# Kernel optimization log

Measured on AMD Instinct MI355X. Metric: run time of the kernel, lower is better.

## Reference

```python
import jax, jax.numpy as jnp
import numpy as np

B, N, H, E, D = 8, 2048, 1024, 8, 2048


def setup_inputs() -> dict:
    key = jax.random.key(0)
    k = jax.random.split(key, 5)
    x = jax.random.normal(k[0], (B, N, H), dtype=jnp.float32)
    Wr = jax.random.normal(k[1], (H, E), dtype=jnp.float32) * 0.02
    br = jnp.zeros((E,), dtype=jnp.float32)
    W1 = jax.random.normal(k[2], (E, H, D), dtype=jnp.float32) * 0.02
    b1 = jnp.zeros((E, D), dtype=jnp.float32)
    W2 = jax.random.normal(k[3], (E, D, H), dtype=jnp.float32) * 0.02
    b2 = jnp.zeros((E, H), dtype=jnp.float32)
    return {"x": x, "Wr": Wr, "br": br, "W1": W1, "b1": b1, "W2": W2, "b2": b2}


def reference(x, Wr, br, W1, b1, W2, b2):
    # x: [B,N,H]; router v1, top-1, eval mode (no expert dropout)
    Bx, Nx, Hx = x.shape
    Ex = Wr.shape[1]
    x_flat = x.reshape(Bx * Nx, Hx)                      # [T,H]
    logits = x_flat @ Wr + br                            # [T,E]
    probs = jax.nn.softmax(logits, axis=-1)              # [T,E]
    expert_idx = jnp.argmax(probs, axis=-1)              # [T]

    out_flat = jnp.zeros_like(x_flat)
    for e in range(Ex):  # small fixed loop over experts
        h = jax.nn.gelu(x_flat @ W1[e] + b1[e], approximate=False)  # exact erf GELU (torch default)
        eout = h @ W2[e] + b2[e]                         # [T,H]
        out_flat = jnp.where((expert_idx == e)[:, None], eout, out_flat)

    out = x + out_flat.reshape(Bx, Nx, Hx)               # residual

    p_i = probs.mean(axis=0)                             # [E]
    balance_loss = Ex * jnp.sum(p_i ** 2)
    EPS = 1e-8
    entropy = -jnp.sum(probs * jnp.log(probs + EPS), axis=-1)
    entropy_loss = entropy.mean()
    tokens_per_expert = jnp.bincount(expert_idx, length=Ex)
    return out, balance_loss, entropy_loss, tokens_per_expert
```

## Files before the change

kernel.cpp:

```cpp
#include <hip/hip_runtime.h>
#include <math.h>

#define TT 16384
#define HH 1024
#define DD 2048
#define EE 8
#define MAXTILES 160

typedef float f32x4 __attribute__((ext_vector_type(4)));
typedef __bf16 bf16x8 __attribute__((ext_vector_type(8)));

__device__ __forceinline__ unsigned short f2bf(float f) {
  union { float f; unsigned u; } v; v.f = f;
  unsigned r = v.u + 0x7FFFu + ((v.u >> 16) & 1u);
  return (unsigned short)(r >> 16);
}

__device__ __forceinline__ void gl2lds16(const unsigned short* g, unsigned short* l) {
  __builtin_amdgcn_global_load_lds(
      (const __attribute__((address_space(1))) void*)g,
      (__attribute__((address_space(3))) void*)l, 16, 0, 0);
}

__global__ void k_init(int* counts, float* probs_sum, float* ent_sum) {
  int t = threadIdx.x;
  if (t < EE) { counts[t] = 0; probs_sum[t] = 0.f; }
  if (t == 0) *ent_sum = 0.f;
}

__global__ __launch_bounds__(256) void k_transpose(const float* __restrict__ src,
                                                   unsigned short* __restrict__ dst,
                                                   int R, int C) {
  __shared__ float tile[32][33];
  int tilesC = C / 32, tilesR = R / 32;
  int bid = blockIdx.x;
  int e = bid / (tilesR * tilesC);
  int rem = bid % (tilesR * tilesC);
  int tr = rem / tilesC, tc = rem % tilesC;
  const float* s = src + (size_t)e * R * C;
  unsigned short* d = dst + (size_t)e * R * C;
  int tx = threadIdx.x & 31, ty = threadIdx.x >> 5;
#pragma unroll
  for (int i = 0; i < 4; ++i)
    tile[ty + i * 8][tx] = s[(size_t)(tr * 32 + ty + i * 8) * C + tc * 32 + tx];
  __syncthreads();
#pragma unroll
  for (int i = 0; i < 4; ++i) {
    int rr = ty + i * 8;
    d[(size_t)(tc * 32 + rr) * R + tr * 32 + tx] = f2bf(tile[tx][rr]);
  }
}

__global__ __launch_bounds__(256) void k_router(const float* __restrict__ x,
                                                const float* __restrict__ Wr,
                                                const float* __restrict__ br,
                                                int* __restrict__ eidx,
                                                float* __restrict__ probs_sum,
                                                float* __restrict__ ent_sum,
                                                int* __restrict__ counts,
                                                unsigned short* __restrict__ xb) {
  __shared__ float s_p[EE];
  __shared__ int   s_c[EE];
  __shared__ float s_e;
  int tid = threadIdx.x;
  if (tid < EE) { s_p[tid] = 0.f; s_c[tid] = 0; }
  if (tid == 0) s_e = 0.f;
  __syncthreads();
  int lane = tid & 63, w = tid >> 6;
  for (int tt = 0; tt < 4; ++tt) {
    int token = blockIdx.x * 16 + w * 4 + tt;
    double acc[EE];
#pragma unroll
    for (int e = 0; e < EE; ++e) acc[e] = 0.0;
    const float* xr = x + (size_t)token * HH;
    unsigned short* xo = xb + (size_t)token * HH;
    for (int i = 0; i < 16; ++i) {
      int hh = i * 64 + lane;
      float xf = xr[hh];
      xo[hh] = f2bf(xf);
      double xv = (double)xf;
      const float* wr = Wr + (size_t)hh * EE;
#pragma unroll
      for (int e = 0; e < EE; ++e) acc[e] += xv * (double)wr[e];
    }
#pragma unroll
    for (int off = 32; off > 0; off >>= 1) {
#pragma unroll
      for (int e = 0; e < EE; ++e) acc[e] += __shfl_down(acc[e], off);
    }
    if (lane == 0) {
      double l[EE];
#pragma unroll
      for (int e = 0; e < EE; ++e) l[e] = acc[e] + (double)br[e];
      double m = l[0]; int am = 0;
#pragma unroll
      for (int e = 1; e < EE; ++e) { if (l[e] > m) { m = l[e]; am = e; } }
      double p[EE]; double s = 0.0;
#pragma unroll
      for (int e = 0; e < EE; ++e) { p[e] = exp(l[e] - m); s += p[e]; }
      double inv = 1.0 / s; double ent = 0.0;
#pragma unroll
      for (int e = 0; e < EE; ++e) { p[e] *= inv; ent -= p[e] * log(p[e] + 1e-8); }
      eidx[token] = am;
#pragma unroll
      for (int e = 0; e < EE; ++e) atomicAdd(&s_p[e], (float)p[e]);
      atomicAdd(&s_e, (float)ent);
      atomicAdd(&s_c[am], 1);
    }
  }
  __syncthreads();
  if (tid < EE) { atomicAdd(&probs_sum[tid], s_p[tid]); atomicAdd(&counts[tid], s_c[tid]); }
  if (tid == 0) atomicAdd(ent_sum, s_e);
}

__global__ void k_scan(const int* counts, const float* probs_sum, const float* ent_sum,
                       int* offsets, int* cursor,
                       int* tileE, int* tileR0, int* tileEnd, int* nTiles,
                       float* out_scalars) {
  if (threadIdx.x != 0) return;
  int off = 0, nt = 0;
  for (int e = 0; e < EE; ++e) {
    offsets[e] = off; cursor[e] = off;
    int c = counts[e];
    for (int r = 0; r < c; r += 128) {
      tileE[nt] = e; tileR0[nt] = off + r; tileEnd[nt] = off + c; ++nt;
    }
    off += c;
  }
  offsets[EE] = off;
  *nTiles = nt;
  float bal = 0.f;
  for (int e = 0; e < EE; ++e) { float pi = probs_sum[e] / (float)TT; bal += pi * pi; }
  out_scalars[0] = (float)EE * bal;
  out_scalars[1] = *ent_sum / (float)TT;
  for (int e = 0; e < EE; ++e) out_scalars[2 + e] = (float)counts[e];
}

__global__ __launch_bounds__(256) void k_perm(const int* __restrict__ eidx,
                                              int* cursor, int* __restrict__ perm) {
  int t = blockIdx.x * 256 + threadIdx.x;
  int lane = threadIdx.x & 63;
  int mye = eidx[t];
  int pos = 0;
#pragma unroll
  for (int e = 0; e < EE; ++e) {
    unsigned long long mask = __ballot(mye == e);
    if (mask == 0ull) continue;
    int leader = __ffsll(mask) - 1;
    int base = 0;
    if (lane == leader) base = atomicAdd(&cursor[e], __popcll(mask));
    base = __shfl(base, leader);
    if (mye == e) pos = base + (int)__popcll(mask & ((1ull << lane) - 1ull));
  }
  perm[pos] = t;
}


__global__ __launch_bounds__(256) void k_gemm1(const unsigned short* __restrict__ xb,
                                               const unsigned short* __restrict__ Wt1,
                                               const float* __restrict__ b1,
                                               const int* __restrict__ perm,
                                               const int* __restrict__ tileE,
                                               const int* __restrict__ tileR0,
                                               const int* __restrict__ tileEnd,
                                               const int* __restrict__ nTiles,
                                               unsigned short* __restrict__ hbuf) {
  int tile = blockIdx.y;
  if (tile >= *nTiles) return;
  int e = tileE[tile], r0 = tileR0[tile], rend = tileEnd[tile];
  int c0 = blockIdx.x * 128;
  __shared__ __align__(16) unsigned short As[128 * 32];
  __shared__ __align__(16) unsigned short Bs[128 * 32];
  int tid = threadIdx.x, lane = tid & 63, w = tid >> 6;
  int wr = w >> 1, wc = w & 1;
  int quad = lane >> 4, l16 = lane & 15;
  int srow = lane >> 2, seg = lane & 3;
  int ar0 = w * 32 + srow, ar1 = ar0 + 16;
  int g0 = r0 + ar0; if (g0 >= rend) g0 = rend - 1;
  int g1 = r0 + ar1; if (g1 >= rend) g1 = rend - 1;
  const unsigned short* aG0 = xb + (size_t)perm[g0] * HH + seg * 8;
  const unsigned short* aG1 = xb + (size_t)perm[g1] * HH + seg * 8;
  const unsigned short* bBase = Wt1 + (size_t)e * ((size_t)DD * HH);
  const unsigned short* bG0 = bBase + (size_t)(c0 + ar0) * HH + seg * 8;
  const unsigned short* bG1 = bBase + (size_t)(c0 + ar1) * HH + seg * 8;
  unsigned short* aL0 = &As[(w * 32 + 0) * 32];
  unsigned short* aL1 = &As[(w * 32 + 16) * 32];
  unsigned short* bL0 = &Bs[(w * 32 + 0) * 32];
  unsigned short* bL1 = &Bs[(w * 32 + 16) * 32];
  f32x4 acc[4][4] = {};
  for (int k0 = 0; k0 < HH; k0 += 32) {
    gl2lds16(aG0 + k0, aL0);
    gl2lds16(aG1 + k0, aL1);
    gl2lds16(bG0 + k0, bL0);
    gl2lds16(bG1 + k0, bL1);
    __syncthreads();
    bf16x8 a[4], b[4];
#pragma unroll
    for (int i = 0; i < 4; ++i)
      a[i] = *(const bf16x8*)&As[(wr * 64 + i * 16 + l16) * 32 + quad * 8];
#pragma unroll
    for (int j = 0; j < 4; ++j)
      b[j] = *(const bf16x8*)&Bs[(wc * 64 + j * 16 + l16) * 32 + quad * 8];
#pragma unroll
    for (int i = 0; i < 4; ++i)
#pragma unroll
      for (int j = 0; j < 4; ++j)
        acc[i][j] = __builtin_amdgcn_mfma_f32_16x16x32_bf16(a[i], b[j], acc[i][j], 0, 0, 0);
    __syncthreads();
  }
  float bias[4];
#pragma unroll
  for (int j = 0; j < 4; ++j) bias[j] = b1[e * DD + c0 + wc * 64 + j * 16 + l16];
#pragma unroll
  for (int i = 0; i < 4; ++i) {
#pragma unroll
    for (int r = 0; r < 4; ++r) {
      int gr = r0 + wr * 64 + i * 16 + quad * 4 + r;
      if (gr < rend) {
#pragma unroll
        for (int j = 0; j < 4; ++j) {
          int col = c0 + wc * 64 + j * 16 + l16;
          float v = acc[i][j][r] + bias[j];
          v = 0.5f * v * (1.0f + erff(v * 0.70710678118654752f));
          hbuf[(size_t)gr * DD + col] = f2bf(v);
        }
      }
    }
  }
}

__global__ __launch_bounds__(256) void k_gemm2(const unsigned short* __restrict__ hbuf,
                                               const unsigned short* __restrict__ Wt2,
                                               const float* __restrict__ b2,
                                               const float* __restrict__ x,
                                               const int* __restrict__ perm,
                                               const int* __restrict__ tileE,
                                               const int* __restrict__ tileR0,
                                               const int* __restrict__ tileEnd,
                                               const int* __restrict__ nTiles,
                                               float* __restrict__ outp) {
  int tile = blockIdx.y;
  if (tile >= *nTiles) return;
  int e = tileE[tile], r0 = tileR0[tile], rend = tileEnd[tile];
  int c0 = blockIdx.x * 128;
  __shared__ __align__(16) unsigned short As[128 * 32];
  __shared__ __align__(16) unsigned short Bs[128 * 32];
  int tid = threadIdx.x, lane = tid & 63, w = tid >> 6;
  int wr = w >> 1, wc = w & 1;
  int quad = lane >> 4, l16 = lane & 15;
  int srow = lane >> 2, seg = lane & 3;
  int ar0 = w * 32 + srow, ar1 = ar0 + 16;
  int g0 = r0 + ar0; if (g0 >= rend) g0 = rend - 1;
  int g1 = r0 + ar1; if (g1 >= rend) g1 = rend - 1;
  const unsigned short* aG0 = hbuf + (size_t)g0 * DD + seg * 8;
  const unsigned short* aG1 = hbuf + (size_t)g1 * DD + seg * 8;
  const unsigned short* bBase = Wt2 + (size_t)e * ((size_t)HH * DD);
  const unsigned short* bG0 = bBase + (size_t)(c0 + ar0) * DD + seg * 8;
  const unsigned short* bG1 = bBase + (size_t)(c0 + ar1) * DD + seg * 8;
  unsigned short* aL0 = &As[(w * 32 + 0) * 32];
  unsigned short* aL1 = &As[(w * 32 + 16) * 32];
  unsigned short* bL0 = &Bs[(w * 32 + 0) * 32];
  unsigned short* bL1 = &Bs[(w * 32 + 16) * 32];
  f32x4 acc[4][4] = {};
  for (int k0 = 0; k0 < DD; k0 += 32) {
    gl2lds16(aG0 + k0, aL0);
    gl2lds16(aG1 + k0, aL1);
    gl2lds16(bG0 + k0, bL0);
    gl2lds16(bG1 + k0, bL1);
    __syncthreads();
    bf16x8 a[4], b[4];
#pragma unroll
    for (int i = 0; i < 4; ++i)
      a[i] = *(const bf16x8*)&As[(wr * 64 + i * 16 + l16) * 32 + quad * 8];
#pragma unroll
    for (int j = 0; j < 4; ++j)
      b[j] = *(const bf16x8*)&Bs[(wc * 64 + j * 16 + l16) * 32 + quad * 8];
#pragma unroll
    for (int i = 0; i < 4; ++i)
#pragma unroll
      for (int j = 0; j < 4; ++j)
        acc[i][j] = __builtin_amdgcn_mfma_f32_16x16x32_bf16(a[i], b[j], acc[i][j], 0, 0, 0);
    __syncthreads();
  }
  float bias[4];
#pragma unroll
  for (int j = 0; j < 4; ++j) bias[j] = b2[e * HH + c0 + wc * 64 + j * 16 + l16];
#pragma unroll
  for (int i = 0; i < 4; ++i) {
#pragma unroll
    for (int r = 0; r < 4; ++r) {
      int gr = r0 + wr * 64 + i * 16 + quad * 4 + r;
      if (gr < rend) {
        int tok = perm[gr];
#pragma unroll
        for (int j = 0; j < 4; ++j) {
          int col = c0 + wc * 64 + j * 16 + l16;
          size_t oi = (size_t)tok * HH + col;
          outp[oi] = x[oi] + bias[j] + acc[i][j][r];
        }
      }
    }
  }
}

extern "C" void kernel_launch(void* const* d_in, const int* in_sizes, int n_in,
                              void* d_out, int out_size, void* d_ws, size_t ws_size,
                              hipStream_t stream) {
  const float* x  = (const float*)d_in[0];
  const float* Wr = (const float*)d_in[1];
  const float* br = (const float*)d_in[2];
  const float* W1 = (const float*)d_in[3];
  const float* b1 = (const float*)d_in[4];
  const float* W2 = (const float*)d_in[5];
  const float* b2 = (const float*)d_in[6];
  float* outp = (float*)d_out;

  char* ws = (char*)d_ws;
  int*   counts    = (int*)(ws + 0);
  int*   cursor    = (int*)(ws + 64);
  int*   nTiles    = (int*)(ws + 128);
  float* probs_sum = (float*)(ws + 192);
  float* ent_sum   = (float*)(ws + 256);
  int*   offsets   = (int*)(ws + 320);
  int*   tileE     = (int*)(ws + 512);
  int*   tileR0    = (int*)(ws + 2048);
  int*   tileEnd   = (int*)(ws + 3584);
  int*   eidx      = (int*)(ws + 8192);
  int*   perm      = (int*)(ws + 8192 + 4 * (size_t)TT);
  size_t off = 8192 + 8 * (size_t)TT;
  unsigned short* xb   = (unsigned short*)(ws + off); off += (size_t)TT * HH * 2;
  unsigned short* Wt1  = (unsigned short*)(ws + off); off += (size_t)EE * DD * HH * 2;
  unsigned short* Wt2  = (unsigned short*)(ws + off); off += (size_t)EE * HH * DD * 2;
  unsigned short* hbuf = (unsigned short*)(ws + off); off += (size_t)TT * DD * 2;

  k_init<<<1, 64, 0, stream>>>(counts, probs_sum, ent_sum);
  k_transpose<<<EE * (HH / 32) * (DD / 32), 256, 0, stream>>>(W1, Wt1, HH, DD);
  k_transpose<<<EE * (DD / 32) * (HH / 32), 256, 0, stream>>>(W2, Wt2, DD, HH);
  k_router<<<TT / 16, 256, 0, stream>>>(x, Wr, br, eidx, probs_sum, ent_sum, counts, xb);
  k_scan<<<1, 64, 0, stream>>>(counts, probs_sum, ent_sum, offsets, cursor,
                               tileE, tileR0, tileEnd, nTiles, outp + (size_t)TT * HH);
  k_perm<<<TT / 256, 256, 0, stream>>>(eidx, cursor, perm);
  dim3 g1(DD / 128, MAXTILES);
  k_gemm1<<<g1, 256, 0, stream>>>(xb, Wt1, b1, perm, tileE, tileR0, tileEnd, nTiles, hbuf);
  dim3 g2(HH / 128, MAXTILES);
  k_gemm2<<<g2, 256, 0, stream>>>(hbuf, Wt2, b2, x, perm, tileE, tileR0, tileEnd, nTiles, outp);
}
```

Measured before the change: 598.3 us.

## Widen GEMM tiles to 128x256 with 512 threads, vectorize transpose and router

Both expert GEMMs now use 128x256 output tiles computed by 8 waves, so each A tile staged in LDS is reused across twice as many columns. The aim is to cut redundant global and L2 traffic on the activation rows. The weight transpose kernel now uses 64x64 tiles with float4 loads, converts to bf16 before the shared-memory stage, and writes vectorized output. The router reads x and Wr as float4. The larger blocks lower grid parallelism and may raise register pressure under the launch bounds of 512 threads with a minimum of 4 blocks.

```diff
diff --git a/kernel.cpp b/kernel.cpp
--- a/kernel.cpp
+++ b/kernel.cpp
@@ -6,6 +6,7 @@
 #define DD 2048
 #define EE 8
 #define MAXTILES 160
+#define BK 32
 
 typedef float f32x4 __attribute__((ext_vector_type(4)));
 typedef __bf16 bf16x8 __attribute__((ext_vector_type(8)));
@@ -31,23 +32,35 @@
 __global__ __launch_bounds__(256) void k_transpose(const float* __restrict__ src,
                                                    unsigned short* __restrict__ dst,
                                                    int R, int C) {
-  __shared__ float tile[32][33];
-  int tilesC = C / 32, tilesR = R / 32;
+  __shared__ unsigned short st[64][72];
+  int tilesC = C / 64, tilesR = R / 64;
   int bid = blockIdx.x;
   int e = bid / (tilesR * tilesC);
   int rem = bid % (tilesR * tilesC);
   int tr = rem / tilesC, tc = rem % tilesC;
   const float* s = src + (size_t)e * R * C;
   unsigned short* d = dst + (size_t)e * R * C;
-  int tx = threadIdx.x & 31, ty = threadIdx.x >> 5;
-#pragma unroll
-  for (int i = 0; i < 4; ++i)
-    tile[ty + i * 8][tx] = s[(size_t)(tr * 32 + ty + i * 8) * C + tc * 32 + tx];
+  int t = threadIdx.x;
+  int rl0 = t >> 4, cl = (t & 15) * 4;
+#pragma unroll
+  for (int i = 0; i < 4; ++i) {
+    int rl = rl0 + i * 16;
+    float4 v = *(const float4*)(s + (size_t)(tr * 64 + rl) * C + tc * 64 + cl);
+    st[cl + 0][rl] = f2bf(v.x);
+    st[cl + 1][rl] = f2bf(v.y);
+    st[cl + 2][rl] = f2bf(v.z);
+    st[cl + 3][rl] = f2bf(v.w);
+  }
   __syncthreads();
-#pragma unroll
-  for (int i = 0; i < 4; ++i) {
-    int rr = ty + i * 8;
-    d[(size_t)(tc * 32 + rr) * R + tr * 32 + tx] = f2bf(tile[tx][rr]);
+  int oc0 = t >> 3, j8 = (t & 7) * 8;
+#pragma unroll
+  for (int i = 0; i < 2; ++i) {
+    int oc = oc0 + i * 32;
+    ushort4 a = *(const ushort4*)&st[oc][j8];
+    ushort4 b = *(const ushort4*)&st[oc][j8 + 4];
+    unsigned short* dp = d + (size_t)(tc * 64 + oc) * R + tr * 64 + j8;
+    *(ushort4*)dp = a;
+    *(ushort4*)(dp + 4) = b;
   }
 }
 
@@ -74,14 +87,24 @@
     for (int e = 0; e < EE; ++e) acc[e] = 0.0;
     const float* xr = x + (size_t)token * HH;
     unsigned short* xo = xb + (size_t)token * HH;
-    for (int i = 0; i < 16; ++i) {
-      int hh = i * 64 + lane;
-      float xf = xr[hh];
-      xo[hh] = f2bf(xf);
-      double xv = (double)xf;
-      const float* wr = Wr + (size_t)hh * EE;
-#pragma unroll
-      for (int e = 0; e < EE; ++e) acc[e] += xv * (double)wr[e];
+#pragma unroll
+    for (int it = 0; it < 4; ++it) {
+      int h0 = it * 256 + lane * 4;
+      float4 xv = *(const float4*)(xr + h0);
+      ushort4 o; o.x = f2bf(xv.x); o.y = f2bf(xv.y); o.z = f2bf(xv.z); o.w = f2bf(xv.w);
+      *(ushort4*)(xo + h0) = o;
+      float xa[4] = {xv.x, xv.y, xv.z, xv.w};
+#pragma unroll
+      for (int j = 0; j < 4; ++j) {
+        const float* wr = Wr + (size_t)(h0 + j) * EE;
+        float4 w0 = *(const float4*)wr;
+        float4 w1 = *(const float4*)(wr + 4);
+        double xd = (double)xa[j];
+        acc[0] += xd * (double)w0.x; acc[1] += xd * (double)w0.y;
+        acc[2] += xd * (double)w0.z; acc[3] += xd * (double)w0.w;
+        acc[4] += xd * (double)w1.x; acc[5] += xd * (double)w1.y;
+        acc[6] += xd * (double)w1.z; acc[7] += xd * (double)w1.w;
+      }
     }
 #pragma unroll
     for (int off = 32; off > 0; off >>= 1) {
@@ -156,51 +179,46 @@
 }
 
 
-__global__ __launch_bounds__(256) void k_gemm1(const unsigned short* __restrict__ xb,
-                                               const unsigned short* __restrict__ Wt1,
-                                               const float* __restrict__ b1,
-                                               const int* __restrict__ perm,
-                                               const int* __restrict__ tileE,
-                                               const int* __restrict__ tileR0,
-                                               const int* __restrict__ tileEnd,
-                                               const int* __restrict__ nTiles,
-                                               unsigned short* __restrict__ hbuf) {
+__global__ __launch_bounds__(512, 4) void k_gemm1(const unsigned short* __restrict__ xb,
+                                                  const unsigned short* __restrict__ Wt1,
+                                                  const float* __restrict__ b1,
+                                                  const int* __restrict__ perm,
+                                                  const int* __restrict__ tileE,
+                                                  const int* __restrict__ tileR0,
+                                                  const int* __restrict__ tileEnd,
+                                                  const int* __restrict__ nTiles,
+                                                  unsigned short* __restrict__ hbuf) {
   int tile = blockIdx.y;
   if (tile >= *nTiles) return;
   int e = tileE[tile], r0 = tileR0[tile], rend = tileEnd[tile];
-  int c0 = blockIdx.x * 128;
-  __shared__ __align__(16) unsigned short As[128 * 32];
-  __shared__ __align__(16) unsigned short Bs[128 * 32];
+  int c0 = blockIdx.x * 256;
+  __shared__ __align__(16) unsigned short As[128 * BK];
+  __shared__ __align__(16) unsigned short Bs[256 * BK];
   int tid = threadIdx.x, lane = tid & 63, w = tid >> 6;
-  int wr = w >> 1, wc = w & 1;
+  int wr = w & 1, wc = w >> 1;
   int quad = lane >> 4, l16 = lane & 15;
-  int srow = lane >> 2, seg = lane & 3;
-  int ar0 = w * 32 + srow, ar1 = ar0 + 16;
-  int g0 = r0 + ar0; if (g0 >= rend) g0 = rend - 1;
-  int g1 = r0 + ar1; if (g1 >= rend) g1 = rend - 1;
-  const unsigned short* aG0 = xb + (size_t)perm[g0] * HH + seg * 8;
-  const unsigned short* aG1 = xb + (size_t)perm[g1] * HH + seg * 8;
+  int srow = lane >> 2, schunk = (lane & 3) * 8;
+  int gA = r0 + w * 16 + srow; if (gA >= rend) gA = rend - 1;
+  const unsigned short* aG = xb + (size_t)perm[gA] * HH + schunk;
+  unsigned short* aL = As + (w * 16) * BK;
   const unsigned short* bBase = Wt1 + (size_t)e * ((size_t)DD * HH);
-  const unsigned short* bG0 = bBase + (size_t)(c0 + ar0) * HH + seg * 8;
-  const unsigned short* bG1 = bBase + (size_t)(c0 + ar1) * HH + seg * 8;
-  unsigned short* aL0 = &As[(w * 32 + 0) * 32];
-  unsigned short* aL1 = &As[(w * 32 + 16) * 32];
-  unsigned short* bL0 = &Bs[(w * 32 + 0) * 32];
-  unsigned short* bL1 = &Bs[(w * 32 + 16) * 32];
+  const unsigned short* bG0 = bBase + (size_t)(c0 + w * 32 + srow) * HH + schunk;
+  const unsigned short* bG1 = bBase + (size_t)(c0 + w * 32 + 16 + srow) * HH + schunk;
+  unsigned short* bL0 = Bs + (w * 32) * BK;
+  unsigned short* bL1 = Bs + (w * 32 + 16) * BK;
   f32x4 acc[4][4] = {};
-  for (int k0 = 0; k0 < HH; k0 += 32) {
-    gl2lds16(aG0 + k0, aL0);
-    gl2lds16(aG1 + k0, aL1);
+  for (int k0 = 0; k0 < HH; k0 += BK) {
+    gl2lds16(aG + k0, aL);
     gl2lds16(bG0 + k0, bL0);
     gl2lds16(bG1 + k0, bL1);
     __syncthreads();
     bf16x8 a[4], b[4];
 #pragma unroll
     for (int i = 0; i < 4; ++i)
-      a[i] = *(const bf16x8*)&As[(wr * 64 + i * 16 + l16) * 32 + quad * 8];
+      a[i] = *(const bf16x8*)&As[(wr * 64 + i * 16 + l16) * BK + quad * 8];
 #pragma unroll
     for (int j = 0; j < 4; ++j)
-      b[j] = *(const bf16x8*)&Bs[(wc * 64 + j * 16 + l16) * 32 + quad * 8];
+      b[j] = *(const bf16x8*)&Bs[(wc * 64 + j * 16 + l16) * BK + quad * 8];
 #pragma unroll
     for (int i = 0; i < 4; ++i)
 #pragma unroll
@@ -229,52 +247,47 @@
   }
 }
 
-__global__ __launch_bounds__(256) void k_gemm2(const unsigned short* __restrict__ hbuf,
-                                               const unsigned short* __restrict__ Wt2,
-                                               const float* __restrict__ b2,
-                                               const float* __restrict__ x,
-                                               const int* __restrict__ perm,
-                                               const int* __restrict__ tileE,
-                                               const int* __restrict__ tileR0,
-                                               const int* __restrict__ tileEnd,
-                                               const int* __restrict__ nTiles,
-                                               float* __restrict__ outp) {
+__global__ __launch_bounds__(512, 4) void k_gemm2(const unsigned short* __restrict__ hbuf,
+                                                  const unsigned short* __restrict__ Wt2,
+                                                  const float* __restrict__ b2,
+                                                  const float* __restrict__ x,
+                                                  const int* __restrict__ perm,
+                                                  const int* __restrict__ tileE,
+                                                  const int* __restrict__ tileR0,
+                                                  const int* __restrict__ tileEnd,
+                                                  const int* __restrict__ nTiles,
+                                                  float* __restrict__ outp) {
   int tile = blockIdx.y;
   if (tile >= *nTiles) return;
   int e = tileE[tile], r0 = tileR0[tile], rend = tileEnd[tile];
-  int c0 = blockIdx.x * 128;
-  __shared__ __align__(16) unsigned short As[128 * 32];
-  __shared__ __align__(16) unsigned short Bs[128 * 32];
+  int c0 = blockIdx.x * 256;
+  __shared__ __align__(16) unsigned short As[128 * BK];
+  __shared__ __align__(16) unsigned short Bs[256 * BK];
   int tid = threadIdx.x, lane = tid & 63, w = tid >> 6;
-  int wr = w >> 1, wc = w & 1;
+  int wr = w & 1, wc = w >> 1;
   int quad = lane >> 4, l16 = lane & 15;
-  int srow = lane >> 2, seg = lane & 3;
-  int ar0 = w * 32 + srow, ar1 = ar0 + 16;
-  int g0 = r0 + ar0; if (g0 >= rend) g0 = rend - 1;
-  int g1 = r0 + ar1; if (g1 >= rend) g1 = rend - 1;
-  const unsigned short* aG0 = hbuf + (size_t)g0 * DD + seg * 8;
-  const unsigned short* aG1 = hbuf + (size_t)g1 * DD + seg * 8;
+  int srow = lane >> 2, schunk = (lane & 3) * 8;
+  int gA = r0 + w * 16 + srow; if (gA >= rend) gA = rend - 1;
+  const unsigned short* aG = hbuf + (size_t)gA * DD + schunk;
+  unsigned short* aL = As + (w * 16) * BK;
   const unsigned short* bBase = Wt2 + (size_t)e * ((size_t)HH * DD);
-  const unsigned short* bG0 = bBase + (size_t)(c0 + ar0) * DD + seg * 8;
-  const unsigned short* bG1 = bBase + (size_t)(c0 + ar1) * DD + seg * 8;
-  unsigned short* aL0 = &As[(w * 32 + 0) * 32];
-  unsigned short* aL1 = &As[(w * 32 + 16) * 32];
-  unsigned short* bL0 = &Bs[(w * 32 + 0) * 32];
-  unsigned short* bL1 = &Bs[(w * 32 + 16) * 32];
+  const unsigned short* bG0 = bBase + (size_t)(c0 + w * 32 + srow) * DD + schunk;
+  const unsigned short* bG1 = bBase + (size_t)(c0 + w * 32 + 16 + srow) * DD + schunk;
+  unsigned short* bL0 = Bs + (w * 32) * BK;
+  unsigned short* bL1 = Bs + (w * 32 + 16) * BK;
   f32x4 acc[4][4] = {};
-  for (int k0 = 0; k0 < DD; k0 += 32) {
-    gl2lds16(aG0 + k0, aL0);
-    gl2lds16(aG1 + k0, aL1);
+  for (int k0 = 0; k0 < DD; k0 += BK) {
+    gl2lds16(aG + k0, aL);
     gl2lds16(bG0 + k0, bL0);
     gl2lds16(bG1 + k0, bL1);
     __syncthreads();
     bf16x8 a[4], b[4];
 #pragma unroll
     for (int i = 0; i < 4; ++i)
-      a[i] = *(const bf16x8*)&As[(wr * 64 + i * 16 + l16) * 32 + quad * 8];
+      a[i] = *(const bf16x8*)&As[(wr * 64 + i * 16 + l16) * BK + quad * 8];
 #pragma unroll
     for (int j = 0; j < 4; ++j)
-      b[j] = *(const bf16x8*)&Bs[(wc * 64 + j * 16 + l16) * 32 + quad * 8];
+      b[j] = *(const bf16x8*)&Bs[(wc * 64 + j * 16 + l16) * BK + quad * 8];
 #pragma unroll
     for (int i = 0; i < 4; ++i)
 #pragma unroll
@@ -334,14 +347,14 @@
   unsigned short* hbuf = (unsigned short*)(ws + off); off += (size_t)TT * DD * 2;
 
   k_init<<<1, 64, 0, stream>>>(counts, probs_sum, ent_sum);
-  k_transpose<<<EE * (HH / 32) * (DD / 32), 256, 0, stream>>>(W1, Wt1, HH, DD);
-  k_transpose<<<EE * (DD / 32) * (HH / 32), 256, 0, stream>>>(W2, Wt2, DD, HH);
+  k_transpose<<<EE * (HH / 64) * (DD / 64), 256, 0, stream>>>(W1, Wt1, HH, DD);
+  k_transpose<<<EE * (DD / 64) * (HH / 64), 256, 0, stream>>>(W2, Wt2, DD, HH);
   k_router<<<TT / 16, 256, 0, stream>>>(x, Wr, br, eidx, probs_sum, ent_sum, counts, xb);
   k_scan<<<1, 64, 0, stream>>>(counts, probs_sum, ent_sum, offsets, cursor,
                                tileE, tileR0, tileEnd, nTiles, outp + (size_t)TT * HH);
   k_perm<<<TT / 256, 256, 0, stream>>>(eidx, cursor, perm);
-  dim3 g1(DD / 128, MAXTILES);
-  k_gemm1<<<g1, 256, 0, stream>>>(xb, Wt1, b1, perm, tileE, tileR0, tileEnd, nTiles, hbuf);
-  dim3 g2(HH / 128, MAXTILES);
-  k_gemm2<<<g2, 256, 0, stream>>>(hbuf, Wt2, b2, x, perm, tileE, tileR0, tileEnd, nTiles, outp);
-}
+  dim3 g1(DD / 256, MAXTILES);
+  k_gemm1<<<g1, 512, 0, stream>>>(xb, Wt1, b1, perm, tileE, tileR0, tileEnd, nTiles, hbuf);
+  dim3 g2(HH / 256, MAXTILES);
+  k_gemm2<<<g2, 512, 0, stream>>>(hbuf, Wt2, b2, x, perm, tileE, tileR0, tileEnd, nTiles, outp);
+}
```

Measured after the change: 619.0 us. +3.5%, slower.
